# Kernel tuning notes

Hardware: AMD Instinct MI355X
Metric: run time of the kernel (lower is better)

The kernel has to match this reference:

```python
import jax, jax.numpy as jnp
import numpy as np

S0 = 192
C = [16, 32, 48, 64, 80]      # nPlanes = m*i, m=16, 5 strides
SL = [192, 96, 48, 24, 12]    # spatial size per level
OFF27 = jnp.asarray(np.stack(np.meshgrid(*([[-1, 0, 1]] * 3), indexing='ij'), -1).reshape(-1, 3), jnp.int32)
OFF8 = jnp.asarray(np.stack(np.meshgrid(*([[0, 1]] * 3), indexing='ij'), -1).reshape(-1, 3), jnp.int32)


def _flat(c, S):
    return (c[..., 0] * S + c[..., 1]) * S + c[..., 2]


def _grid(coords, S):
    g = jnp.full((S * S * S,), -1, jnp.int32)
    return g.at[_flat(coords, S)].set(jnp.arange(coords.shape[0], dtype=jnp.int32))


def _subconv(feat, coords, grid, S, W):
    # submanifold 3x3x3 conv over active sites only; W: [27, a, b]
    nb = coords[:, None, :] + OFF27                      # [N,27,3]
    valid = jnp.all((nb >= 0) & (nb < S), axis=-1)
    idx = grid[_flat(jnp.clip(nb, 0, S - 1), S)]         # [N,27]
    valid = valid & (idx >= 0)
    g = jnp.where(valid[..., None], feat[jnp.maximum(idx, 0)], 0.0)
    return jnp.einsum('nka,kab->nb', g, W)


def _downconv(feat, grid_f, S_f, out_coords, W):
    # kernel-2 stride-2 sparse conv; W: [8, a, b]
    src = out_coords[:, None, :] * 2 + OFF8              # [M,8,3]
    valid = jnp.all(src < S_f, axis=-1)
    idx = grid_f[_flat(src, S_f)]
    valid = valid & (idx >= 0)
    g = jnp.where(valid[..., None], feat[jnp.maximum(idx, 0)], 0.0)
    return jnp.einsum('nka,kab->nb', g, W)


def _bnrelu(x, g, b, eps=1e-4):
    # BatchNormLeakyReLU(leakiness=0) == BN (batch stats over active sites) + ReLU
    mu = jnp.mean(x, 0)
    var = jnp.mean((x - mu) ** 2, 0)
    return jax.nn.relu((x - mu) * jax.lax.rsqrt(var + eps) * g + b)


def _unpool(feat_c, grid_c, S_c, fine_coords, k):
    # UnPooling x k levels: copy coarse parent feature to each fine active site
    return feat_c[grid_c[_flat(fine_coords // (1 << k), S_c)]]


def _selection(scores):
    return (jax.nn.softmax(scores, axis=1)[:, 1:2] > 0.5).astype(scores.dtype)


def _forward(coords, features, w_in, blk_w, blk_g, blk_b, dn_g, dn_b, dn_w,
             ppn1_w, ppn1_sw, ppn2_w, ppn2_sw, ppn3_w, ppn3_pw, ppn3_sw):
    grids = [_grid(coords[l], SL[l]) for l in range(5)]
    x = _subconv(features, coords[0], grids[0], SL[0], w_in)   # input layer
    fmaps = [x]
    for i in range(4):  # encoder levels with residual blocks + downsample
        for r in range(2):
            h = _bnrelu(x, blk_g[i][2 * r], blk_b[i][2 * r])
            h = _subconv(h, coords[i], grids[i], SL[i], blk_w[i][2 * r])
            h = _bnrelu(h, blk_g[i][2 * r + 1], blk_b[i][2 * r + 1])
            h = _subconv(h, coords[i], grids[i], SL[i], blk_w[i][2 * r + 1])
            x = x + h  # ConcatTable(Identity, conv path) + AddTable, a==b
        x = _downconv(_bnrelu(x, dn_g[i], dn_b[i]), grids[i], SL[i], coords[i + 1], dn_w[i])
        fmaps.append(x)
    x = _subconv(x, coords[4], grids[4], SL[4], ppn1_w)
    ppn1_scores = x @ ppn1_sw                                   # 1x1 conv
    att1 = _unpool(_selection(ppn1_scores), grids[4], SL[4], coords[2], 2)
    y = fmaps[2] * att1                                         # Multiply at half_stride
    y = _subconv(y, coords[2], grids[2], SL[2], ppn2_w)
    ppn2_scores = y @ ppn2_sw
    att2 = _unpool(_selection(ppn2_scores), grids[2], SL[2], coords[0], 2)
    z = fmaps[0] * att2
    z = _subconv(z, coords[0], grids[0], SL[0], ppn3_w)
    out0 = jnp.concatenate([z @ ppn3_pw, z @ ppn3_sw], axis=1)
    out1 = jnp.concatenate([coords[4].astype(out0.dtype), ppn1_scores], axis=1)
    out2 = jnp.concatenate([coords[2].astype(out0.dtype), ppn2_scores], axis=1)
    return out0, out1, out2


def _make_coords():
    rng = np.random.RandomState(0)
    c0 = np.unique(rng.randint(0, S0, size=(100000, 3)), axis=0).astype(np.int32)
    cs = [c0]
    for _ in range(4):
        cs.append(np.unique(cs[-1] // 2, axis=0).astype(np.int32))
    return cs


def setup_inputs():
    key = jax.random.key(0)
    ks = iter(jax.random.split(key, 64))
    cs = _make_coords()
    inp = {f'coords{l}': jnp.asarray(cs[l]) for l in range(5)}
    N0 = cs[0].shape[0]
    inp['features'] = jax.random.normal(next(ks), (N0, 1), jnp.float32)

    def w(k, shape, fan):
        return jax.random.normal(k, shape, jnp.float32) * (fan ** -0.5)

    inp['w_in'] = w(next(ks), (27, 1, C[0]), 27)
    for i in range(4):
        inp[f'blk_w{i}'] = w(next(ks), (4, 27, C[i], C[i]), 27 * C[i])
        inp[f'blk_g{i}'] = jnp.ones((4, C[i]), jnp.float32)
        inp[f'blk_b{i}'] = jnp.zeros((4, C[i]), jnp.float32)
        inp[f'dn_g{i}'] = jnp.ones((C[i],), jnp.float32)
        inp[f'dn_b{i}'] = jnp.zeros((C[i],), jnp.float32)
        inp[f'dn_w{i}'] = w(next(ks), (8, C[i], C[i + 1]), 8 * C[i])
    inp['ppn1_w'] = w(next(ks), (27, C[4], C[4]), 27 * C[4])
    inp['ppn1_sw'] = w(next(ks), (C[4], 2), C[4])
    inp['ppn2_w'] = w(next(ks), (27, C[2], C[2]), 27 * C[2])
    inp['ppn2_sw'] = w(next(ks), (C[2], 2), C[2])
    inp['ppn3_w'] = w(next(ks), (27, C[0], C[0]), 27 * C[0])
    inp['ppn3_pw'] = w(next(ks), (C[0], 3), C[0])
    inp['ppn3_sw'] = w(next(ks), (C[0], 2), C[0])
    return inp


def reference(features, w_in,
              blk_w0, blk_g0, blk_b0, dn_g0, dn_b0, dn_w0,
              blk_w1, blk_g1, blk_b1, dn_g1, dn_b1, dn_w1,
              blk_w2, blk_g2, blk_b2, dn_g2, dn_b2, dn_w2,
              blk_w3, blk_g3, blk_b3, dn_g3, dn_b3, dn_w3,
              ppn1_w, ppn1_sw, ppn2_w, ppn2_sw, ppn3_w, ppn3_pw, ppn3_sw,
              coords0, coords1, coords2, coords3, coords4):
    coords = [coords0, coords1, coords2, coords3, coords4]
    return _forward(coords, features, w_in,
                    [blk_w0, blk_w1, blk_w2, blk_w3],
                    [blk_g0, blk_g1, blk_g2, blk_g3],
                    [blk_b0, blk_b1, blk_b2, blk_b3],
                    [dn_g0, dn_g1, dn_g2, dn_g3],
                    [dn_b0, dn_b1, dn_b2, dn_b3],
                    [dn_w0, dn_w1, dn_w2, dn_w3],
                    ppn1_w, ppn1_sw, ppn2_w, ppn2_sw, ppn3_w, ppn3_pw, ppn3_sw)
```

## Files before the change

kernel.cpp:

```cpp
#include <hip/hip_runtime.h>
#include <cstdint>
#include <cstddef>

#define TPB 256

typedef _Float16 f16x8 __attribute__((ext_vector_type(8)));
typedef float f32x4 __attribute__((ext_vector_type(4)));

__device__ __forceinline__ void block_sync_lds() {
    asm volatile("s_waitcnt lgkmcnt(0)" ::: "memory");
    __builtin_amdgcn_sched_barrier(0);
    __builtin_amdgcn_s_barrier();
    __builtin_amdgcn_sched_barrier(0);
}


static __global__ void kscatter(int* __restrict__ grid, const int* __restrict__ coords,
                                int N, int S) {
    int i = blockIdx.x * blockDim.x + threadIdx.x;
    if (i >= N) return;
    int x = coords[3 * i], y = coords[3 * i + 1], z = coords[3 * i + 2];
    grid[(x * S + y) * S + z] = i;
}

static __global__ void knbr27(int* __restrict__ nbr, const int* __restrict__ coords,
                              const int* __restrict__ grid, int N, int S, int zr) {
    int t = blockIdx.x * blockDim.x + threadIdx.x;
    if (t >= N * 27) return;
    int n = t / 27, k = t - 27 * n;
    int x = coords[3 * n]     + (k / 9) - 1;
    int y = coords[3 * n + 1] + ((k / 3) % 3) - 1;
    int z = coords[3 * n + 2] + (k % 3) - 1;
    int v = -1;
    if ((unsigned)x < (unsigned)S && (unsigned)y < (unsigned)S && (unsigned)z < (unsigned)S)
        v = grid[(x * S + y) * S + z];
    nbr[t] = (v < 0) ? zr : v;
}

static __global__ void kdown8(int* __restrict__ dn, const int* __restrict__ coords,
                              const int* __restrict__ grid, int M, int S_f, int zr) {
    int t = blockIdx.x * blockDim.x + threadIdx.x;
    if (t >= M * 8) return;
    int n = t >> 3, k = t & 7;
    int x = coords[3 * n] * 2     + ((k >> 2) & 1);
    int y = coords[3 * n + 1] * 2 + ((k >> 1) & 1);
    int z = coords[3 * n + 2] * 2 + (k & 1);
    int v = grid[(x * S_f + y) * S_f + z];
    dn[t] = (v < 0) ? zr : v;
}

static __global__ void kup(int* __restrict__ up, const int* __restrict__ cf,
                           const int* __restrict__ gc, int N, int Sc) {
    int n = blockIdx.x * blockDim.x + threadIdx.x;
    if (n >= N) return;
    int x = cf[3 * n] >> 2, y = cf[3 * n + 1] >> 2, z = cf[3 * n + 2] >> 2;
    up[n] = gc[(x * Sc + y) * Sc + z];
}

static __global__ void ksplitw(_Float16* __restrict__ dst, const float* __restrict__ src,
                               int KREAL, int KPAD, int A, int B) {
    int t = blockIdx.x * blockDim.x + threadIdx.x;
    if (t >= KPAD * A * B) return;
    int a = t % A;
    int b = (t / A) % B;
    int k = t / (A * B);
    float v = (k < KREAL) ? src[((size_t)k * A + a) * B + b] : 0.0f;
    _Float16 hi = (_Float16)v;
    _Float16 lo = (_Float16)(v - (float)hi);
    size_t row = ((size_t)k * B + b) * (size_t)(2 * A);
    dst[row + a] = hi;
    dst[row + A + a] = lo;
}


static __global__ void kstats(double* __restrict__ st, const float* __restrict__ x,
                              int N, int C) {
    extern __shared__ double sh[];
    int tid = threadIdx.x;
    int c = tid % C, rl = tid / C;
    double s = 0.0, q = 0.0;
    int base = blockIdx.x * 256 + rl * 64;
    for (int it = 0; it < 64; it++) {
        int r = base + it;
        if (r < N) {
            double v = (double)x[(size_t)r * C + c];
            s += v;
            q = fma(v, v, q);
        }
    }
    double* ss = sh;
    double* sq = sh + 4 * C;
    ss[tid] = s; sq[tid] = q;
    __syncthreads();
    if (tid < C) {
        double S = ss[tid] + ss[tid + C] + ss[tid + 2 * C] + ss[tid + 3 * C];
        double Q = sq[tid] + sq[tid + C] + sq[tid + 2 * C] + sq[tid + 3 * C];
        atomicAdd(&st[tid], S);
        atomicAdd(&st[80 + tid], Q);
    }
}

static __global__ void kbnrelu_h(_Float16* __restrict__ y, const float4* __restrict__ x,
                                 const double* __restrict__ st, const float* __restrict__ g,
                                 const float* __restrict__ b, int N, int C) {
    __shared__ float sc[80], bh[80];
    int tid = threadIdx.x;
    if (tid < C) {
        double invN = 1.0 / (double)N;
        double S = 0.0, Q = 0.0;
#pragma unroll
        for (int c = 0; c < 16; c++) {
            S += st[c * 160 + tid];
            Q += st[c * 160 + 80 + tid];
        }
        double mu = S * invN;
        double var = Q * invN - mu * mu;
        float s = g[tid] * rsqrtf((float)var + 1e-4f);
        sc[tid] = s;
        bh[tid] = b[tid] - (float)mu * s;
    }
    __syncthreads();
    int C8 = C >> 3;
    int chunks = (N + 1) * C8;
    int t = blockIdx.x * blockDim.x + tid;
    if (t >= chunks) return;
    int n = t / C8, cc = t - n * C8;
    f16x8 hi = {}, lo = {};
    if (n < N) {
        float4 q0 = x[n * (C >> 2) + cc * 2];
        float4 q1 = x[n * (C >> 2) + cc * 2 + 1];
        float v[8] = {q0.x, q0.y, q0.z, q0.w, q1.x, q1.y, q1.z, q1.w};
#pragma unroll
        for (int j = 0; j < 8; j++) {
            float r = fmaxf(fmaf(v[j], sc[cc * 8 + j], bh[cc * 8 + j]), 0.0f);
            _Float16 h = (_Float16)r;
            hi[j] = h;
            lo[j] = (_Float16)(r - (float)h);
        }
    }
    *(f16x8*)&y[(size_t)n * 2 * C + cc * 16] = hi;
    *(f16x8*)&y[(size_t)n * 2 * C + cc * 16 + 8] = lo;
}

static __global__ void kcvt_h(_Float16* __restrict__ y, const float4* __restrict__ x,
                              int N, int C) {
    int C8 = C >> 3;
    int t = blockIdx.x * blockDim.x + threadIdx.x;
    if (t >= (N + 1) * C8) return;
    int n = t / C8, cc = t - n * C8;
    f16x8 hi = {}, lo = {};
    if (n < N) {
        float4 q0 = x[n * (C >> 2) + cc * 2];
        float4 q1 = x[n * (C >> 2) + cc * 2 + 1];
        float v[8] = {q0.x, q0.y, q0.z, q0.w, q1.x, q1.y, q1.z, q1.w};
#pragma unroll
        for (int j = 0; j < 8; j++) {
            _Float16 h = (_Float16)v[j];
            hi[j] = h;
            lo[j] = (_Float16)(v[j] - (float)h);
        }
    }
    *(f16x8*)&y[(size_t)n * 2 * C + cc * 16] = hi;
    *(f16x8*)&y[(size_t)n * 2 * C + cc * 16 + 8] = lo;
}

static __global__ void kmulatt_h(_Float16* __restrict__ y, const float4* __restrict__ fmap,
                                 const int* __restrict__ up, const float* __restrict__ sc,
                                 int N, int C) {
    int C8 = C >> 3;
    int t = blockIdx.x * blockDim.x + threadIdx.x;
    if (t >= (N + 1) * C8) return;
    int n = t / C8, cc = t - n * C8;
    f16x8 hi = {}, lo = {};
    if (n < N) {
        int p = up[n];
        float att = (sc[2 * p + 1] > sc[2 * p]) ? 1.0f : 0.0f;
        float4 q0 = fmap[n * (C >> 2) + cc * 2];
        float4 q1 = fmap[n * (C >> 2) + cc * 2 + 1];
        float v[8] = {q0.x, q0.y, q0.z, q0.w, q1.x, q1.y, q1.z, q1.w};
#pragma unroll
        for (int j = 0; j < 8; j++) {
            float r = v[j] * att;
            _Float16 h = (_Float16)r;
            hi[j] = h;
            lo[j] = (_Float16)(r - (float)h);
        }
    }
    *(f16x8*)&y[(size_t)n * 2 * C + cc * 16] = hi;
    *(f16x8*)&y[(size_t)n * 2 * C + cc * 16 + 8] = lo;
}


template <int A, int B, int TAPS, int TPI, int TR, int MT, int KG, bool ADD>
__launch_bounds__(256, 2)
static __global__ void kconvmf(float* __restrict__ out, const _Float16* __restrict__ feat,
                               const int* __restrict__ nbr, const _Float16* __restrict__ Wsp,
                               const float* __restrict__ res, double* __restrict__ stp,
                               int N, int zr) {
    constexpr int NT_W = B / 16;
    static_assert(TR == 4 * MT * 16, "tile/wave mismatch");
    constexpr int KPT = (TPI == 1) ? ((A + 31) & ~31)
                      : (TPI == 2) ? ((A + 15) & ~15)
                                   : ((A + 7) & ~7);
    constexpr int KT = TPI * KPT;
    static_assert(KT % 32 == 0, "KT must be multiple of 32");
    constexpr int KSTEPS = KT / 32;
    constexpr int KTCH = KT / 8;
    constexpr int PKT = (KTCH == 12) ? 16 : KTCH;
    static_assert(PKT == 8 || PKT == 16, "bad PKT");
    constexpr int RH = PKT * 8;
    constexpr int QQ = KPT / 8;
    constexpr int AQ = A / 8;
    constexpr int A2 = 2 * A;
    constexpr int ITERS = (TAPS + TPI - 1) / TPI;
    constexpr int IPG = (ITERS + KG - 1) / KG;
    constexpr int WROWS = 2 * B;
    constexpr int WSBH = WROWS * RH;
    constexpr int WTOT = WROWS * KTCH;
    constexpr int WPT = (WTOT + 255) / 256;

    __shared__ __attribute__((aligned(16))) _Float16 wsb[WSBH];
    __shared__ double sred[(KG == 1) ? 4 * 2 * B : 1];

    const int tid = threadIdx.x;

    int bx;
    {
        int nwg = gridDim.x, bid = blockIdx.x;
        int q = nwg >> 3, r = nwg & 7, xcd = bid & 7, ix = bid >> 3;
        bx = (xcd < r) ? xcd * (q + 1) + ix : r * (q + 1) + (xcd - r) * q + ix;
    }
    const int row0 = bx * TR;
    const int it0 = (KG > 1) ? blockIdx.y * IPG : 0;
    const int it1 = (KG > 1) ? ((it0 + IPG < ITERS) ? it0 + IPG : ITERS) : ITERS;

    const int lane = tid & 63, wid = tid >> 6;
    const int lrow = lane & 15, lgrp = lane >> 4;
    const int mb = wid * MT * 16;

    int w_lds[WPT], w_off[WPT];
    bool w_ok[WPT], w_real[WPT];
#pragma unroll
    for (int i = 0; i < WPT; i++) {
        int task = tid + i * 256;
        bool ok = (WTOT % 256 == 0) || (task < WTOT);
        int tc = ok ? task : 0;
        int q = tc % KTCH;
        int row = tc / KTCH;
        int bcol = row % B, pp = row / B;
        int t = q / QQ, qq = q - t * QQ;
        w_lds[i] = row * RH + (q ^ (row & (PKT - 1))) * 8;
        w_off[i] = (t * B + bcol) * A2 + pp * A + qq * 8;
        w_ok[i] = ok;
        w_real[i] = ok && (qq < AQ);
    }
    int rowm[MT];
#pragma unroll
    for (int mt = 0; mt < MT; mt++) rowm[mt] = row0 + mb + mt * 16 + lrow;

    f32x4 acc[MT][NT_W];
#pragma unroll
    for (int mt = 0; mt < MT; mt++)
#pragma unroll
        for (int nt = 0; nt < NT_W; nt++)
            acc[mt][nt] = (f32x4){0.f, 0.f, 0.f, 0.f};

    int nidA[MT][TPI], nidB[MT][TPI];
    f16x8 faA[MT][KSTEPS][2], faB[MT][KSTEPS][2];
    f16x8 wg[WPT];

    auto loadnbr = [&](auto& nd, int it) {
        int tb = it * TPI;
#pragma unroll
        for (int mt = 0; mt < MT; mt++)
#pragma unroll
            for (int t = 0; t < TPI; t++)
                nd[mt][t] = (rowm[mt] < N && tb + t < TAPS)
                          ? nbr[(size_t)rowm[mt] * TAPS + tb + t] : zr;
    };
    auto loadA = [&](auto& fd, const auto& nd) {
#pragma unroll
        for (int mt = 0; mt < MT; mt++)
#pragma unroll
            for (int ks = 0; ks < KSTEPS; ks++) {
                int qc = ks * 4 + lgrp;
                int t = qc / QQ;
                int cq = qc - t * QQ;
                int id;
                if constexpr (TPI == 1) id = nd[mt][0];
                else if constexpr (TPI == 2) id = (t == 0) ? nd[mt][0] : nd[mt][1];
                else {
                    int lo2 = (t == 0) ? nd[mt][0] : nd[mt][1];
                    int hi2 = (t == 2) ? nd[mt][2] : nd[mt][3];
                    id = (t < 2) ? lo2 : hi2;
                }
                const _Float16* p = feat + (size_t)id * A2 + cq * 16;
                if constexpr (QQ > AQ) {
                    bool okc = (cq < AQ);
                    fd[mt][ks][0] = okc ? *(const f16x8*)p : (f16x8){};
                    fd[mt][ks][1] = okc ? *(const f16x8*)(p + 8) : (f16x8){};
                } else {
                    fd[mt][ks][0] = *(const f16x8*)p;
                    fd[mt][ks][1] = *(const f16x8*)(p + 8);
                }
            }
    };
    auto loadW = [&](int it) {
        size_t base = (size_t)it * TPI * B * A2;
#pragma unroll
        for (int i = 0; i < WPT; i++)
            wg[i] = w_real[i] ? *(const f16x8*)&Wsp[base + w_off[i]] : (f16x8){};
    };
    auto storeW = [&]() {
#pragma unroll
        for (int i = 0; i < WPT; i++)
            if (w_ok[i]) *(f16x8*)&wsb[w_lds[i]] = wg[i];
    };
    auto domfma = [&](const auto& fd) {
#pragma unroll
        for (int ks = 0; ks < KSTEPS; ++ks) {
            const int qc = ks * 4 + lgrp;
            f16x8 bh[NT_W], bl[NT_W];
#pragma unroll
            for (int nt = 0; nt < NT_W; ++nt) {
                int rH = nt * 16 + lrow;
                bh[nt] = *(const f16x8*)&wsb[rH * RH + (qc ^ (rH & (PKT - 1))) * 8];
                int rL = B + rH;
                bl[nt] = *(const f16x8*)&wsb[rL * RH + (qc ^ (rL & (PKT - 1))) * 8];
            }
#pragma unroll
            for (int mt = 0; mt < MT; ++mt)
#pragma unroll
                for (int nt = 0; nt < NT_W; ++nt) {
                    acc[mt][nt] = __builtin_amdgcn_mfma_f32_16x16x32_f16(fd[mt][ks][0], bh[nt], acc[mt][nt], 0, 0, 0);
                    acc[mt][nt] = __builtin_amdgcn_mfma_f32_16x16x32_f16(fd[mt][ks][1], bh[nt], acc[mt][nt], 0, 0, 0);
                    acc[mt][nt] = __builtin_amdgcn_mfma_f32_16x16x32_f16(fd[mt][ks][0], bl[nt], acc[mt][nt], 0, 0, 0);
                }
        }
    };

    loadnbr(nidA, it0);
    loadA(faA, nidA);
    loadW(it0);
    storeW();
    if (it0 + 1 < it1) loadnbr(nidB, it0 + 1);
    block_sync_lds();
    if (it0 + 1 < it1) loadW(it0 + 1);

    auto body = [&](const auto& fc, auto& fn, auto& ncur, const auto& nnx, int it) {
        const bool m1 = (it + 1 < it1), m2 = (it + 2 < it1);
        if (m1) loadA(fn, nnx);
        if (m2) loadnbr(ncur, it + 2);
        domfma(fc);
        if (m1) {
            block_sync_lds();
            storeW();
            if (m2) loadW(it + 2);
            block_sync_lds();
        }
    };
    for (int it = it0; it < it1; ) {
        body(faA, faB, nidA, nidB, it); ++it;
        if (it >= it1) break;
        body(faB, faA, nidB, nidA, it); ++it;
    }

    const bool dostats = (stp != nullptr);
    double ssum[NT_W], sqs[NT_W];
#pragma unroll
    for (int nt = 0; nt < NT_W; nt++) { ssum[nt] = 0.0; sqs[nt] = 0.0; }
#pragma unroll
    for (int mt = 0; mt < MT; ++mt) {
        int gr0 = row0 + mb + mt * 16 + lgrp * 4;
#pragma unroll
        for (int nt = 0; nt < NT_W; ++nt) {
            int gc = nt * 16 + lrow;
#pragma unroll
            for (int j = 0; j < 4; ++j) {
                int r = gr0 + j;
                if (r < N) {
                    size_t o = (size_t)r * B + gc;
                    if (KG > 1) {
                        atomicAdd(&out[o], acc[mt][nt][j]);
                    } else {
                        float v = acc[mt][nt][j];
                        if (ADD) v += res[o];
                        out[o] = v;
                        if (dostats) {
                            double dv = (double)v;
                            ssum[nt] += dv;
                            sqs[nt] = fma(dv, dv, sqs[nt]);
                        }
                    }
                }
            }
        }
    }
    if (KG == 1) {
        if (dostats) {
#pragma unroll
            for (int nt = 0; nt < NT_W; nt++) {
                ssum[nt] += __shfl_xor(ssum[nt], 16, 64);
                ssum[nt] += __shfl_xor(ssum[nt], 32, 64);
                sqs[nt] += __shfl_xor(sqs[nt], 16, 64);
                sqs[nt] += __shfl_xor(sqs[nt], 32, 64);
            }
            if (lgrp == 0) {
#pragma unroll
                for (int nt = 0; nt < NT_W; nt++) {
                    sred[(wid * 2 + 0) * B + nt * 16 + lrow] = ssum[nt];
                    sred[(wid * 2 + 1) * B + nt * 16 + lrow] = sqs[nt];
                }
            }
            __syncthreads();
            if (wid == 0) {
                double* sb = stp + (bx & 15) * 160;
                for (int c = lane; c < B; c += 64) {
                    double S = sred[c] + sred[2 * B + c] + sred[4 * B + c] + sred[6 * B + c];
                    double Q = sred[B + c] + sred[3 * B + c] + sred[5 * B + c] + sred[7 * B + c];
                    atomicAdd(&sb[c], S);
                    atomicAdd(&sb[80 + c], Q);
                }
            }
        }
    }
}

static __global__ void kconv_in(float* __restrict__ out, const float* __restrict__ f,
                                const int* __restrict__ nbr, const float* __restrict__ W,
                                int N, int zr) {
    int t = blockIdx.x * blockDim.x + threadIdx.x;
    if (t >= N * 4) return;
    int n = t >> 2, bq = t & 3;
    float4 acc = make_float4(0.f, 0.f, 0.f, 0.f);
    const float4* W4 = (const float4*)W;
    for (int k = 0; k < 27; k++) {
        int id = nbr[n * 27 + k];
        if (id == zr) continue;
        float v = f[id];
        float4 w = W4[k * 4 + bq];
        acc.x = fmaf(v, w.x, acc.x);
        acc.y = fmaf(v, w.y, acc.y);
        acc.z = fmaf(v, w.z, acc.z);
        acc.w = fmaf(v, w.w, acc.w);
    }
    ((float4*)out)[n * 4 + bq] = acc;
}


static __global__ void kscores(float* __restrict__ sc, const float* __restrict__ x,
                               const float* __restrict__ w, int N, int C) {
    int n = blockIdx.x * blockDim.x + threadIdx.x;
    if (n >= N) return;
    float s0 = 0.0f, s1 = 0.0f;
    const float* xr = x + (size_t)n * C;
    for (int c = 0; c < C; c++) {
        float v = xr[c];
        s0 = fmaf(v, w[2 * c], s0);
        s1 = fmaf(v, w[2 * c + 1], s1);
    }
    sc[2 * n] = s0;
    sc[2 * n + 1] = s1;
}

static __global__ void kout0(float* __restrict__ out, const float* __restrict__ z,
                             const float* __restrict__ pw, const float* __restrict__ sw,
                             int N) {
    int n = blockIdx.x * blockDim.x + threadIdx.x;
    if (n >= N) return;
    float o0 = 0, o1 = 0, o2 = 0, o3 = 0, o4 = 0;
    const float* zr = z + (size_t)n * 16;
#pragma unroll
    for (int c = 0; c < 16; c++) {
        float v = zr[c];
        o0 = fmaf(v, pw[3 * c], o0);
        o1 = fmaf(v, pw[3 * c + 1], o1);
        o2 = fmaf(v, pw[3 * c + 2], o2);
        o3 = fmaf(v, sw[2 * c], o3);
        o4 = fmaf(v, sw[2 * c + 1], o4);
    }
    float* r = out + (size_t)n * 5;
    r[0] = o0; r[1] = o1; r[2] = o2; r[3] = o3; r[4] = o4;
}

static __global__ void koutc(float* __restrict__ out, const int* __restrict__ coords,
                             const float* __restrict__ sc, int N) {
    int n = blockIdx.x * blockDim.x + threadIdx.x;
    if (n >= N) return;
    float* r = out + (size_t)n * 5;
    r[0] = (float)coords[3 * n];
    r[1] = (float)coords[3 * n + 1];
    r[2] = (float)coords[3 * n + 2];
    r[3] = sc[2 * n];
    r[4] = sc[2 * n + 1];
}


static inline int cdiv(long a, int b) { return (int)((a + b - 1) / b); }

static void conv(hipStream_t s, float* out, const _Float16* feat, const int* nbr,
                 const _Float16* Wsp, const float* res, double* stp,
                 int N, int A, int B, int TAPS, int zr) {
#define CASE(AA, BB, TT, TPI_, TR_, MT_, KG_)                                              \
    else if (A == AA && B == BB && TAPS == TT) {                                           \
        if (KG_ > 1 && !res) hipMemsetAsync(out, 0, (size_t)N * BB * 4, s);                \
        dim3 g(cdiv(N, TR_), KG_), blk(256);                                               \
        if (res) kconvmf<AA, BB, TT, TPI_, TR_, MT_, KG_, true><<<g, blk, 0, s>>>(out, feat, nbr, Wsp, res, stp, N, zr); \
        else     kconvmf<AA, BB, TT, TPI_, TR_, MT_, KG_, false><<<g, blk, 0, s>>>(out, feat, nbr, Wsp, nullptr, stp, N, zr); \
    }
    if (false) {}
    CASE(16, 16, 27,  4,  64,  1, 1)
    CASE(32, 32, 27,  2,  64,  1, 1)
    CASE(48, 48, 27,  2,  64,  1, 1)
    CASE(64, 64, 27,  1,  64,  1, 4)
    CASE(80, 80, 27,  1,  64,  1, 9)
    CASE(16, 32,  8,  4,  64,  1, 1)
    CASE(32, 48,  8,  2,  64,  1, 1)
    CASE(48, 64,  8,  2,  64,  1, 2)
    CASE(64, 80,  8,  1,  64,  1, 4)
#undef CASE
}

static void bnapply(hipStream_t s, _Float16* out, const float* x, double* st,
                    const float* g, const float* b, int N, int C, bool pre) {
    if (!pre)
        kstats<<<cdiv(N, 256), 4 * C, 8 * C * 2 * sizeof(double), s>>>(st, x, N, C);
    int chunks = (N + 1) * (C / 8);
    kbnrelu_h<<<cdiv(chunks, 256), 256, 0, s>>>(out, (const float4*)x, st, g, b, N, C);
}

extern "C" void kernel_launch(void* const* d_in, const int* in_sizes, int n_in,
                              void* d_out, int out_size, void* d_ws, size_t ws_size,
                              hipStream_t stream) {
    (void)n_in; (void)out_size; (void)ws_size;
    const int SL[5] = {192, 96, 48, 24, 12};
    const int C[5] = {16, 32, 48, 64, 80};
    int N[5];
    const int* coords[5];
    for (int l = 0; l < 5; l++) { N[l] = in_sizes[l] / 3; coords[l] = (const int*)d_in[l]; }
    const float* features = (const float*)d_in[5];
    const float* w_in = (const float*)d_in[6];
    const float *blk_w[4], *blk_g[4], *blk_b[4], *dn_g[4], *dn_b[4], *dn_w[4];
    for (int i = 0; i < 4; i++) {
        blk_w[i] = (const float*)d_in[7 + 6 * i];
        blk_g[i] = (const float*)d_in[8 + 6 * i];
        blk_b[i] = (const float*)d_in[9 + 6 * i];
        dn_g[i] = (const float*)d_in[10 + 6 * i];
        dn_b[i] = (const float*)d_in[11 + 6 * i];
        dn_w[i] = (const float*)d_in[12 + 6 * i];
    }
    const float* ppn1_w  = (const float*)d_in[31];
    const float* ppn1_sw = (const float*)d_in[32];
    const float* ppn2_w  = (const float*)d_in[33];
    const float* ppn2_sw = (const float*)d_in[34];
    const float* ppn3_w  = (const float*)d_in[35];
    const float* ppn3_pw = (const float*)d_in[36];
    const float* ppn3_sw = (const float*)d_in[37];
    float* dout = (float*)d_out;

    char* ws = (char*)d_ws;
    size_t off = 0;
    auto alloc = [&](size_t bytes) -> char* {
        off = (off + 255) & ~(size_t)255;
        char* p = ws + off;
        off += bytes;
        return p;
    };
    int* nbr[5];
    for (int l = 0; l < 5; l++) nbr[l] = (int*)alloc((size_t)N[l] * 27 * 4);
    int* down8[4];
    for (int i = 0; i < 4; i++) down8[i] = (int*)alloc((size_t)N[i + 1] * 8 * 4);
    int* up1 = (int*)alloc((size_t)N[2] * 4);
    int* up2 = (int*)alloc((size_t)N[0] * 4);
    double* stats = (double*)alloc((size_t)26 * 2560 * sizeof(double));
    _Float16* blkWsp[4];
    _Float16* dnWsp[4];
    for (int i = 0; i < 4; i++) {
        blkWsp[i] = (_Float16*)alloc((size_t)4 * 28 * C[i] * 2 * C[i] * 2);
        dnWsp[i] = (_Float16*)alloc((size_t)8 * C[i + 1] * 2 * C[i] * 2);
    }
    _Float16* p1Wsp = (_Float16*)alloc((size_t)27 * 80 * 160 * 2);
    _Float16* p2Wsp = (_Float16*)alloc((size_t)28 * 48 * 96 * 2);
    _Float16* p3Wsp = (_Float16*)alloc((size_t)28 * 16 * 32 * 2);
    float* fmap0 = (float*)alloc((size_t)N[0] * 16 * 4);
    float* fmap2 = (float*)alloc((size_t)N[2] * 48 * 4);
    float* sc1 = (float*)alloc((size_t)N[4] * 2 * 4);
    float* sc2 = (float*)alloc((size_t)N[2] * 2 * 4);

    size_t BIG = 0;
    for (int l = 0; l < 5; l++) {
        size_t s = (size_t)(N[l] + 1) * C[l] * 4;
        if (s > BIG) BIG = s;
    }
    BIG = (BIG + 255) & ~(size_t)255;
    off = (off + 255) & ~(size_t)255;
    size_t trans = off;
    int* grid[5];
    size_t gtot = 0;
    for (int l = 0; l < 5; l++) {
        grid[l] = (int*)(ws + trans + gtot);
        gtot += (size_t)SL[l] * SL[l] * SL[l] * 4;
    }
    float* B0 = (float*)(ws + trans);
    float* B1 = (float*)(ws + trans + BIG);
    float* B2 = (float*)(ws + trans + 2 * BIG);

    hipMemsetAsync(ws + trans, 0xFF, gtot, stream);
    hipMemsetAsync(stats, 0, (size_t)26 * 2560 * sizeof(double), stream);
    for (int l = 0; l < 5; l++)
        kscatter<<<cdiv(N[l], TPB), TPB, 0, stream>>>(grid[l], coords[l], N[l], SL[l]);
    for (int l = 0; l < 5; l++)
        knbr27<<<cdiv((long)N[l] * 27, TPB), TPB, 0, stream>>>(nbr[l], coords[l], grid[l], N[l], SL[l], N[l]);
    for (int i = 0; i < 4; i++)
        kdown8<<<cdiv((long)N[i + 1] * 8, TPB), TPB, 0, stream>>>(down8[i], coords[i + 1], grid[i], N[i + 1], SL[i], N[i]);
    kup<<<cdiv(N[2], TPB), TPB, 0, stream>>>(up1, coords[2], grid[4], N[2], 12);
    kup<<<cdiv(N[0], TPB), TPB, 0, stream>>>(up2, coords[0], grid[2], N[0], 48);
    for (int i = 0; i < 4; i++) {
        int Ci = C[i];
        for (int c = 0; c < 4; c++) {
            int n1 = 28 * Ci * Ci;
            ksplitw<<<cdiv(n1, TPB), TPB, 0, stream>>>(
                blkWsp[i] + (size_t)c * 28 * Ci * 2 * Ci,
                blk_w[i] + (size_t)c * 27 * Ci * Ci, 27, 28, Ci, Ci);
        }
        int n2 = 8 * Ci * C[i + 1];
        ksplitw<<<cdiv(n2, TPB), TPB, 0, stream>>>(dnWsp[i], dn_w[i], 8, 8, Ci, C[i + 1]);
    }
    ksplitw<<<cdiv(28 * 6400, TPB), TPB, 0, stream>>>(p1Wsp, ppn1_w, 27, 27, 80, 80);
    ksplitw<<<cdiv(28 * 2304, TPB), TPB, 0, stream>>>(p2Wsp, ppn2_w, 27, 28, 48, 48);
    ksplitw<<<cdiv(28 * 256, TPB), TPB, 0, stream>>>(p3Wsp, ppn3_w, 27, 28, 16, 16);

    int slot = 0;
    auto stn = [&]() { return stats + 2560 * (slot++); };
    auto stpeek = [&]() { return stats + 2560 * slot; };

    float* curX = B0;
    kconv_in<<<cdiv((long)N[0] * 4, TPB), TPB, 0, stream>>>(curX, features, nbr[0], w_in, N[0], N[0]);
    hipMemcpyAsync(fmap0, curX, (size_t)N[0] * 16 * 4, hipMemcpyDeviceToDevice, stream);

    auto others = [&](float* cur, float*& t1, float*& t2) {
        if (cur == B0) { t1 = B1; t2 = B2; }
        else if (cur == B1) { t1 = B0; t2 = B2; }
        else { t1 = B0; t2 = B1; }
    };

    bool entryPre = false;
    for (int i = 0; i < 4; i++) {
        int Ni = N[i], Ci = C[i];
        float *T1, *T2;
        others(curX, T1, T2);
        size_t wsl = (size_t)28 * Ci * 2 * Ci;
        bool fuseL = (i < 3);
        for (int r = 0; r < 2; r++) {
            bnapply(stream, (_Float16*)T1, curX, stn(), blk_g[i] + (2 * r) * Ci,
                    blk_b[i] + (2 * r) * Ci, Ni, Ci, r == 0 ? entryPre : fuseL);
            conv(stream, T2, (const _Float16*)T1, nbr[i], blkWsp[i] + (2 * r) * wsl,
                 nullptr, fuseL ? stpeek() : nullptr, Ni, Ci, Ci, 27, Ni);
            bnapply(stream, (_Float16*)T1, T2, stn(), blk_g[i] + (2 * r + 1) * Ci,
                    blk_b[i] + (2 * r + 1) * Ci, Ni, Ci, fuseL);
            conv(stream, curX, (const _Float16*)T1, nbr[i], blkWsp[i] + (2 * r + 1) * wsl,
                 curX, fuseL ? stpeek() : nullptr, Ni, Ci, Ci, 27, Ni);
        }
        bnapply(stream, (_Float16*)T1, curX, stn(), dn_g[i], dn_b[i], Ni, Ci, fuseL);
        bool fuseD = (i < 2);
        conv(stream, T2, (const _Float16*)T1, down8[i], dnWsp[i], nullptr,
             fuseD ? stpeek() : nullptr, N[i + 1], Ci, C[i + 1], 8, Ni);
        entryPre = fuseD;
        if (i == 1)
            hipMemcpyAsync(fmap2, T2, (size_t)N[2] * 48 * 4, hipMemcpyDeviceToDevice, stream);
        curX = T2;
    }

    float *T1, *T2;
    others(curX, T1, T2);
    kcvt_h<<<cdiv((N[4] + 1) * 10, TPB), TPB, 0, stream>>>((_Float16*)T1, (const float4*)curX, N[4], 80);
    conv(stream, T2, (const _Float16*)T1, nbr[4], p1Wsp, nullptr, nullptr, N[4], 80, 80, 27, N[4]);
    kscores<<<cdiv(N[4], TPB), TPB, 0, stream>>>(sc1, T2, ppn1_sw, N[4], 80);
    koutc<<<cdiv(N[4], TPB), TPB, 0, stream>>>(dout + (size_t)N[0] * 5, coords[4], sc1, N[4]);
    kmulatt_h<<<cdiv((long)(N[2] + 1) * 6, TPB), TPB, 0, stream>>>((_Float16*)curX, (const float4*)fmap2, up1, sc1, N[2], 48);
    conv(stream, T1, (const _Float16*)curX, nbr[2], p2Wsp, nullptr, nullptr, N[2], 48, 48, 27, N[2]);
    kscores<<<cdiv(N[2], TPB), TPB, 0, stream>>>(sc2, T1, ppn2_sw, N[2], 48);
    koutc<<<cdiv(N[2], TPB), TPB, 0, stream>>>(dout + (size_t)(N[0] + N[4]) * 5, coords[2], sc2, N[2]);
    kmulatt_h<<<cdiv((long)(N[0] + 1) * 2, TPB), TPB, 0, stream>>>((_Float16*)T2, (const float4*)fmap0, up2, sc2, N[0], 16);
    conv(stream, curX, (const _Float16*)T2, nbr[0], p3Wsp, nullptr, nullptr, N[0], 16, 16, 27, N[0]);
    kout0<<<cdiv(N[0], TPB), TPB, 0, stream>>>(dout, curX, ppn3_pw, ppn3_sw, N[0]);
}
```

Before: 1.258 ms.

## Pre-permute weights and stream them into double-buffered LDS via global_load_lds

The weight split kernel now writes fp16 hi/lo weights already in the swizzled LDS tile layout, one contiguous tile per iteration. The conv kernel then copies each tile straight into LDS with global_load_lds into a double buffer. This replaces the register-staged load/store and removes one barrier per iteration, overlapping the next weight tile fetch with the current MFMA work. The cost is twice the LDS for weights and a hand-tuned vmcnt wait count that must match the number of outstanding loads.

```diff
diff --git a/kernel.cpp b/kernel.cpp
--- a/kernel.cpp
+++ b/kernel.cpp
@@ -6,6 +6,8 @@
 
 typedef _Float16 f16x8 __attribute__((ext_vector_type(8)));
 typedef float f32x4 __attribute__((ext_vector_type(4)));
+typedef const __attribute__((address_space(1))) void* gp1_t;
+typedef __attribute__((address_space(3))) void* lp3_t;
 
 __device__ __forceinline__ void block_sync_lds() {
     asm volatile("s_waitcnt lgkmcnt(0)" ::: "memory");
@@ -57,19 +59,26 @@
     up[n] = gc[(x * Sc + y) * Sc + z];
 }
 
-static __global__ void ksplitw(_Float16* __restrict__ dst, const float* __restrict__ src,
-                               int KREAL, int KPAD, int A, int B) {
-    int t = blockIdx.x * blockDim.x + threadIdx.x;
-    if (t >= KPAD * A * B) return;
-    int a = t % A;
-    int b = (t / A) % B;
-    int k = t / (A * B);
-    float v = (k < KREAL) ? src[((size_t)k * A + a) * B + b] : 0.0f;
+static __global__ void ksplitw_perm(_Float16* __restrict__ dst, const float* __restrict__ src,
+                                    int TAPS, int TPI, int QQ, int KTCH, int PKT,
+                                    int A, int B, int WSBH, long total) {
+    long t = (long)blockIdx.x * blockDim.x + threadIdx.x;
+    if (t >= total) return;
+    int it = (int)(t / WSBH);
+    int r = (int)(t - (long)it * WSBH);
+    int s = r >> 3, j = r & 7;
+    int row = s / PKT, pq = s - row * PKT;
+    int q = pq ^ (row & (PKT - 1));
+    float v = 0.0f;
+    if (q < KTCH) {
+        int tq = q / QQ, qq = q - tq * QQ;
+        int k = it * TPI + tq;
+        int a = qq * 8 + j;
+        if (k < TAPS && a < A)
+            v = src[((size_t)k * A + a) * B + (row % B)];
+    }
     _Float16 hi = (_Float16)v;
-    _Float16 lo = (_Float16)(v - (float)hi);
-    size_t row = ((size_t)k * B + b) * (size_t)(2 * A);
-    dst[row + a] = hi;
-    dst[row + A + a] = lo;
+    dst[t] = (row >= B) ? (_Float16)(v - (float)hi) : hi;
 }
 
 
@@ -216,10 +225,11 @@
     constexpr int IPG = (ITERS + KG - 1) / KG;
     constexpr int WROWS = 2 * B;
     constexpr int WSBH = WROWS * RH;
-    constexpr int WTOT = WROWS * KTCH;
-    constexpr int WPT = (WTOT + 255) / 256;
-
-    __shared__ __attribute__((aligned(16))) _Float16 wsb[WSBH];
+    constexpr int WPW = (WSBH / 8) / 256;
+    static_assert(WPW * 256 * 8 == WSBH, "W tile must split into 1KB wave loads");
+    constexpr int NWAIT = KSTEPS * 2;
+
+    __shared__ __attribute__((aligned(16))) _Float16 wsb[2 * WSBH];
     __shared__ double sred[(KG == 1) ? 4 * 2 * B : 1];
 
     const int tid = threadIdx.x;
@@ -238,22 +248,6 @@
     const int lrow = lane & 15, lgrp = lane >> 4;
     const int mb = wid * MT * 16;
 
-    int w_lds[WPT], w_off[WPT];
-    bool w_ok[WPT], w_real[WPT];
-#pragma unroll
-    for (int i = 0; i < WPT; i++) {
-        int task = tid + i * 256;
-        bool ok = (WTOT % 256 == 0) || (task < WTOT);
-        int tc = ok ? task : 0;
-        int q = tc % KTCH;
-        int row = tc / KTCH;
-        int bcol = row % B, pp = row / B;
-        int t = q / QQ, qq = q - t * QQ;
-        w_lds[i] = row * RH + (q ^ (row & (PKT - 1))) * 8;
-        w_off[i] = (t * B + bcol) * A2 + pp * A + qq * 8;
-        w_ok[i] = ok;
-        w_real[i] = ok && (qq < AQ);
-    }
     int rowm[MT];
 #pragma unroll
     for (int mt = 0; mt < MT; mt++) rowm[mt] = row0 + mb + mt * 16 + lrow;
@@ -267,7 +261,6 @@
 
     int nidA[MT][TPI], nidB[MT][TPI];
     f16x8 faA[MT][KSTEPS][2], faB[MT][KSTEPS][2];
-    f16x8 wg[WPT];
 
     auto loadnbr = [&](auto& nd, int it) {
         int tb = it * TPI;
@@ -305,18 +298,14 @@
                 }
             }
     };
-    auto loadW = [&](int it) {
-        size_t base = (size_t)it * TPI * B * A2;
-#pragma unroll
-        for (int i = 0; i < WPT; i++)
-            wg[i] = w_real[i] ? *(const f16x8*)&Wsp[base + w_off[i]] : (f16x8){};
+    auto issueW = [&](int buf, int it) {
+        const _Float16* src = Wsp + (size_t)it * WSBH + ((size_t)(wid * WPW) * 64 + lane) * 8;
+        _Float16* dst = wsb + buf * WSBH + (wid * WPW) * 512;
+#pragma unroll
+        for (int i = 0; i < WPW; i++)
+            __builtin_amdgcn_global_load_lds((gp1_t)(src + i * 512), (lp3_t)(dst + i * 512), 16, 0, 0);
     };
-    auto storeW = [&]() {
-#pragma unroll
-        for (int i = 0; i < WPT; i++)
-            if (w_ok[i]) *(f16x8*)&wsb[w_lds[i]] = wg[i];
-    };
-    auto domfma = [&](const auto& fd) {
+    auto domfma = [&](const auto& fd, int cb) {
 #pragma unroll
         for (int ks = 0; ks < KSTEPS; ++ks) {
             const int qc = ks * 4 + lgrp;
@@ -324,9 +313,9 @@
 #pragma unroll
             for (int nt = 0; nt < NT_W; ++nt) {
                 int rH = nt * 16 + lrow;
-                bh[nt] = *(const f16x8*)&wsb[rH * RH + (qc ^ (rH & (PKT - 1))) * 8];
+                bh[nt] = *(const f16x8*)&wsb[cb + rH * RH + (qc ^ (rH & (PKT - 1))) * 8];
                 int rL = B + rH;
-                bl[nt] = *(const f16x8*)&wsb[rL * RH + (qc ^ (rL & (PKT - 1))) * 8];
+                bl[nt] = *(const f16x8*)&wsb[cb + rL * RH + (qc ^ (rL & (PKT - 1))) * 8];
             }
 #pragma unroll
             for (int mt = 0; mt < MT; ++mt)
@@ -340,24 +329,29 @@
     };
 
     loadnbr(nidA, it0);
+    issueW(0, it0);
     loadA(faA, nidA);
-    loadW(it0);
-    storeW();
     if (it0 + 1 < it1) loadnbr(nidB, it0 + 1);
+    __builtin_amdgcn_sched_barrier(0);
+    asm volatile("s_waitcnt vmcnt(0)" ::: "memory");
+    __builtin_amdgcn_sched_barrier(0);
     block_sync_lds();
-    if (it0 + 1 < it1) loadW(it0 + 1);
-
+    if (it0 + 1 < it1) issueW(1, it0 + 1);
+
+    int cur = 0;
     auto body = [&](const auto& fc, auto& fn, auto& ncur, const auto& nnx, int it) {
         const bool m1 = (it + 1 < it1), m2 = (it + 2 < it1);
+        if (m2) loadnbr(ncur, it + 2);
         if (m1) loadA(fn, nnx);
-        if (m2) loadnbr(ncur, it + 2);
-        domfma(fc);
+        domfma(fc, cur * WSBH);
         if (m1) {
+            __builtin_amdgcn_sched_barrier(0);
+            asm volatile("s_waitcnt vmcnt(%0)" :: "i"(NWAIT) : "memory");
+            __builtin_amdgcn_sched_barrier(0);
             block_sync_lds();
-            storeW();
-            if (m2) loadW(it + 2);
-            block_sync_lds();
-        }
+            if (m2) issueW(cur, it + 2);
+        }
+        cur ^= 1;
     };
     for (int it = it0; it < it1; ) {
         body(faA, faB, nidA, nidB, it); ++it;
@@ -498,6 +492,26 @@
 
 static inline int cdiv(long a, int b) { return (int)((a + b - 1) / b); }
 
+struct WGeom { int tpi, kpt, ktch, pkt, wsbh, iters; size_t halves; };
+static WGeom wgeom(int A, int B, int TAPS, int tpi) {
+    WGeom g; g.tpi = tpi;
+    g.kpt = (tpi == 1) ? ((A + 31) & ~31) : (tpi == 2) ? ((A + 15) & ~15) : ((A + 7) & ~7);
+    int kt = tpi * g.kpt;
+    g.ktch = kt / 8;
+    g.pkt = (g.ktch == 12) ? 16 : g.ktch;
+    g.wsbh = 2 * B * g.pkt * 8;
+    g.iters = (TAPS + tpi - 1) / tpi;
+    g.halves = (size_t)g.wsbh * g.iters;
+    return g;
+}
+
+static void splitw(hipStream_t s, _Float16* dst, const float* src, int A, int B,
+                   int TAPS, const WGeom& g) {
+    long total = (long)g.halves;
+    ksplitw_perm<<<cdiv(total, TPB), TPB, 0, s>>>(dst, src, TAPS, g.tpi, g.kpt / 8,
+                                                  g.ktch, g.pkt, A, B, g.wsbh, total);
+}
+
 static void conv(hipStream_t s, float* out, const _Float16* feat, const int* nbr,
                  const _Float16* Wsp, const float* res, double* stp,
                  int N, int A, int B, int TAPS, int zr) {
@@ -535,6 +549,8 @@
     (void)n_in; (void)out_size; (void)ws_size;
     const int SL[5] = {192, 96, 48, 24, 12};
     const int C[5] = {16, 32, 48, 64, 80};
+    const int TPI_SUB[4] = {4, 2, 2, 1};
+    const int TPI_DN[4] = {4, 2, 2, 1};
     int N[5];
     const int* coords[5];
     for (int l = 0; l < 5; l++) { N[l] = in_sizes[l] / 3; coords[l] = (const int*)d_in[l]; }
@@ -557,6 +573,15 @@
     const float* ppn3_pw = (const float*)d_in[36];
     const float* ppn3_sw = (const float*)d_in[37];
     float* dout = (float*)d_out;
+
+    WGeom gsub[4], gdn[4];
+    for (int i = 0; i < 4; i++) {
+        gsub[i] = wgeom(C[i], C[i], 27, TPI_SUB[i]);
+        gdn[i] = wgeom(C[i], C[i + 1], 8, TPI_DN[i]);
+    }
+    WGeom gp1 = wgeom(80, 80, 27, 1);
+    WGeom gp2 = wgeom(48, 48, 27, 2);
+    WGeom gp3 = wgeom(16, 16, 27, 4);
 
     char* ws = (char*)d_ws;
     size_t off = 0;
@@ -576,12 +601,12 @@
     _Float16* blkWsp[4];
     _Float16* dnWsp[4];
     for (int i = 0; i < 4; i++) {
-        blkWsp[i] = (_Float16*)alloc((size_t)4 * 28 * C[i] * 2 * C[i] * 2);
-        dnWsp[i] = (_Float16*)alloc((size_t)8 * C[i + 1] * 2 * C[i] * 2);
-    }
-    _Float16* p1Wsp = (_Float16*)alloc((size_t)27 * 80 * 160 * 2);
-    _Float16* p2Wsp = (_Float16*)alloc((size_t)28 * 48 * 96 * 2);
-    _Float16* p3Wsp = (_Float16*)alloc((size_t)28 * 16 * 32 * 2);
+        blkWsp[i] = (_Float16*)alloc(4 * gsub[i].halves * 2);
+        dnWsp[i] = (_Float16*)alloc(gdn[i].halves * 2);
+    }
+    _Float16* p1Wsp = (_Float16*)alloc(gp1.halves * 2);
+    _Float16* p2Wsp = (_Float16*)alloc(gp2.halves * 2);
+    _Float16* p3Wsp = (_Float16*)alloc(gp3.halves * 2);
     float* fmap0 = (float*)alloc((size_t)N[0] * 16 * 4);
     float* fmap2 = (float*)alloc((size_t)N[2] * 48 * 4);
     float* sc1 = (float*)alloc((size_t)N[4] * 2 * 4);
@@ -616,19 +641,14 @@
     kup<<<cdiv(N[2], TPB), TPB, 0, stream>>>(up1, coords[2], grid[4], N[2], 12);
     kup<<<cdiv(N[0], TPB), TPB, 0, stream>>>(up2, coords[0], grid[2], N[0], 48);
     for (int i = 0; i < 4; i++) {
-        int Ci = C[i];
-        for (int c = 0; c < 4; c++) {
-            int n1 = 28 * Ci * Ci;
-            ksplitw<<<cdiv(n1, TPB), TPB, 0, stream>>>(
-                blkWsp[i] + (size_t)c * 28 * Ci * 2 * Ci,
-                blk_w[i] + (size_t)c * 27 * Ci * Ci, 27, 28, Ci, Ci);
-        }
-        int n2 = 8 * Ci * C[i + 1];
-        ksplitw<<<cdiv(n2, TPB), TPB, 0, stream>>>(dnWsp[i], dn_w[i], 8, 8, Ci, C[i + 1]);
-    }
-    ksplitw<<<cdiv(28 * 6400, TPB), TPB, 0, stream>>>(p1Wsp, ppn1_w, 27, 27, 80, 80);
-    ksplitw<<<cdiv(28 * 2304, TPB), TPB, 0, stream>>>(p2Wsp, ppn2_w, 27, 28, 48, 48);
-    ksplitw<<<cdiv(28 * 256, TPB), TPB, 0, stream>>>(p3Wsp, ppn3_w, 27, 28, 16, 16);
+        for (int c = 0; c < 4; c++)
+            splitw(stream, blkWsp[i] + (size_t)c * gsub[i].halves,
+                   blk_w[i] + (size_t)c * 27 * C[i] * C[i], C[i], C[i], 27, gsub[i]);
+        splitw(stream, dnWsp[i], dn_w[i], C[i], C[i + 1], 8, gdn[i]);
+    }
+    splitw(stream, p1Wsp, ppn1_w, 80, 80, 27, gp1);
+    splitw(stream, p2Wsp, ppn2_w, 48, 48, 27, gp2);
+    splitw(stream, p3Wsp, ppn3_w, 16, 16, 27, gp3);
 
     int slot = 0;
     auto stn = [&]() { return stats + 2560 * (slot++); };
@@ -649,16 +669,15 @@
         int Ni = N[i], Ci = C[i];
         float *T1, *T2;
         others(curX, T1, T2);
-        size_t wsl = (size_t)28 * Ci * 2 * Ci;
         bool fuseL = (i < 3);
         for (int r = 0; r < 2; r++) {
             bnapply(stream, (_Float16*)T1, curX, stn(), blk_g[i] + (2 * r) * Ci,
                     blk_b[i] + (2 * r) * Ci, Ni, Ci, r == 0 ? entryPre : fuseL);
-            conv(stream, T2, (const _Float16*)T1, nbr[i], blkWsp[i] + (2 * r) * wsl,
+            conv(stream, T2, (const _Float16*)T1, nbr[i], blkWsp[i] + (size_t)(2 * r) * gsub[i].halves,
                  nullptr, fuseL ? stpeek() : nullptr, Ni, Ci, Ci, 27, Ni);
             bnapply(stream, (_Float16*)T1, T2, stn(), blk_g[i] + (2 * r + 1) * Ci,
                     blk_b[i] + (2 * r + 1) * Ci, Ni, Ci, fuseL);
-            conv(stream, curX, (const _Float16*)T1, nbr[i], blkWsp[i] + (2 * r + 1) * wsl,
+            conv(stream, curX, (const _Float16*)T1, nbr[i], blkWsp[i] + (size_t)(2 * r + 1) * gsub[i].halves,
                  curX, fuseL ? stpeek() : nullptr, Ni, Ci, Ci, 27, Ni);
         }
         bnapply(stream, (_Float16*)T1, curX, stn(), dn_g[i], dn_b[i], Ni, Ci, fuseL);
```

After: 1.286 ms. 2.2% more time.
